# Kernel optimization log

Hardware: AMD Instinct MI355X
Metric: run time of the kernel (lower is better)

## Reference

```python
import jax, jax.numpy as jnp
import numpy as np

B, C, H, W = 4, 64, 128, 128
CO, K, PAD, STRIDE = 64, 3, 1, 1


def setup_inputs() -> dict:
    key = jax.random.key(0)
    k1, k2, k3 = jax.random.split(key, 3)
    x = jax.random.normal(k1, (B, C, H, W), dtype=jnp.float32)
    # small offset weights so predicted offsets stay near the regular grid
    w_off = jax.random.normal(k2, (2 * K * K, C, K, K), dtype=jnp.float32) * 0.01
    b_off = jnp.zeros((2 * K * K,), dtype=jnp.float32)
    w_def = jax.random.normal(k3, (CO, C, K, K), dtype=jnp.float32) * (1.0 / np.sqrt(C * K * K))
    return {"x": x, "w_off": w_off, "b_off": b_off, "w_def": w_def}


def _deform_forward(x, w_off, b_off, w_def):
    Bs, Cs, Hs, Ws = x.shape
    Co = w_def.shape[0]
    KK = K * K
    # offset conv: [B, 2*K*K, Ho, Wo]
    off = jax.lax.conv_general_dilated(
        x, w_off, (STRIDE, STRIDE), [(PAD, PAD), (PAD, PAD)],
        dimension_numbers=("NCHW", "OIHW", "NCHW"))
    off = off + b_off[None, :, None, None]
    Ho, Wo = off.shape[2], off.shape[3]
    off = off.reshape(Bs, KK, 2, Ho, Wo)  # channel 2k -> dy, 2k+1 -> dx
    ky = (jnp.arange(KK) // K).astype(x.dtype)
    kx = (jnp.arange(KK) % K).astype(x.dtype)
    gy = (jnp.arange(Ho) * STRIDE - PAD).astype(x.dtype)
    gx = (jnp.arange(Wo) * STRIDE - PAD).astype(x.dtype)
    # sampling positions per (batch, tap, out_y, out_x)
    py = off[:, :, 0] + ky[None, :, None, None] + gy[None, None, :, None]
    px = off[:, :, 1] + kx[None, :, None, None] + gx[None, None, None, :]
    y0 = jnp.floor(py)
    x0 = jnp.floor(px)
    dy = py - y0
    dx = px - x0
    y0i = y0.astype(jnp.int32)
    x0i = x0.astype(jnp.int32)
    xf = x.reshape(Bs, Cs, Hs * Ws)

    def gather(iy, ix):
        valid = (iy >= 0) & (iy < Hs) & (ix >= 0) & (ix < Ws)
        idx = jnp.clip(iy, 0, Hs - 1) * Ws + jnp.clip(ix, 0, Ws - 1)  # [B,KK,Ho,Wo]
        g = jax.vmap(lambda xb, ib: jnp.take(xb, ib.reshape(-1), axis=1))(xf, idx)
        g = g.reshape(Bs, Cs, KK, Ho, Wo)
        return g * valid[:, None].astype(x.dtype)

    # bilinear sample with zero padding outside the image (torchvision semantics)
    sampled = gather(y0i, x0i) * ((1 - dy) * (1 - dx))[:, None]
    sampled = sampled + gather(y0i, x0i + 1) * ((1 - dy) * dx)[:, None]
    sampled = sampled + gather(y0i + 1, x0i) * (dy * (1 - dx))[:, None]
    sampled = sampled + gather(y0i + 1, x0i + 1) * (dy * dx)[:, None]
    # conv-style weighted accumulation over (channel, tap)
    return jnp.einsum("bckhw,ock->bohw", sampled, w_def.reshape(Co, Cs, KK))


def reference(x, w_off, b_off, w_def):
    return _deform_forward(x, w_off, b_off, w_def)
```

## Files before the change

### kernel.cpp

```cpp
#include <hip/hip_runtime.h>
#include <math.h>


typedef short  v4s __attribute__((ext_vector_type(4)));
typedef short  v8s __attribute__((ext_vector_type(8)));
typedef float  v4f __attribute__((ext_vector_type(4)));
typedef float  v2f __attribute__((ext_vector_type(2)));

namespace {
constexpr int Bn = 4, Cn = 64, Hn = 128, Wn = 128, COn = 64;
constexpr int HWn = 16384;
constexpr int CKn = 576;
constexpr int TILE = 16;
constexpr int RS = 580;
constexpr int HW2 = 132;
constexpr int XPITCH = HW2 * 16;
constexpr size_t XH_OFF   = 0;
constexpr size_t ASWZ_OFF = 2230272;
constexpr size_t AOFF_OFF = ASWZ_OFF + 18432;
constexpr size_t OFFG_OFF = AOFF_OFF + 9216;
}

__device__ __forceinline__ unsigned short f2bf(float f) {
    union { float f; unsigned int u; } v; v.f = f;
    unsigned int u = v.u;
    u += 0x7fffu + ((u >> 16) & 1u);
    return (unsigned short)(u >> 16);
}
__device__ __forceinline__ unsigned int pack2bf(float a, float b) {
    return (unsigned int)f2bf(a) | ((unsigned int)f2bf(b) << 16);
}
__device__ __forceinline__ v2f unpk(unsigned int u) {
    v2f r;
    r.x = __uint_as_float(u << 16);
    r.y = __uint_as_float(u & 0xffff0000u);
    return r;
}

__global__ __launch_bounds__(256) void k_pre(const float* __restrict__ x,
                                             const float* __restrict__ w_def,
                                             const float* __restrict__ w_off,
                                             unsigned int* __restrict__ xh,
                                             unsigned short* __restrict__ aswz,
                                             unsigned short* __restrict__ aoff) {
    const int blk = blockIdx.x;
    const int tid = threadIdx.x;
    if (blk < 1024) {
        __shared__ float tile[64][65];
        const int lane = tid & 63;
        const int grp  = tid >> 6;
        const int b    = blk >> 8;
        const int hw0  = (blk & 255) << 6;
#pragma unroll
        for (int r = 0; r < 16; ++r) {
            const int c = (r << 2) + grp;
            tile[c][lane] = x[(b * Cn + c) * HWn + hw0 + lane];
        }
        __syncthreads();
        const int h = lane >> 5;
        const int m = lane & 31;
#pragma unroll
        for (int r = 0; r < 8; ++r) {
            const int hwl = (r << 3) + (grp << 1) + h;
            const int hw  = hw0 + hwl;
            const int yy  = hw >> 7;
            const int xx  = hw & (Wn - 1);
            const unsigned int u = pack2bf(tile[2 * m][hwl], tile[2 * m + 1][hwl]);
            xh[((size_t)(b * HW2 + yy + 2) * HW2 + (xx + 2)) * 32 + m] = u;
        }
    } else if (blk < 1240) {
        const int idx = (blk - 1024) * 256 + tid;
        if (idx < 36864) {
            const int j = idx & 7;
            const int l = (idx >> 3) & 63;
            const int s = (idx >> 9) % 18;
            const int r = idx / 9216;
            const int co = 16 * r + (l & 15);
            const int kk = 32 * s + 4 * (l >> 4) + (j & 3) + 16 * (j >> 2);
            const int tap = kk >> 6, c = kk & 63;
            aswz[idx] = f2bf(w_def[co * CKn + c * 9 + tap]);
        } else {
            const int i2 = idx - 36864;
            const int j = i2 & 7;
            const int l = (i2 >> 3) & 63;
            const int s = (i2 >> 9) % 18;
            const int r = i2 / 9216;
            const int co = 16 * r + (l & 15);
            const int kk = 32 * s + 4 * (l >> 4) + (j & 3) + 16 * (j >> 2);
            const int tap = kk >> 6, c = kk & 63;
            aoff[i2] = (co < 18) ? f2bf(w_off[co * CKn + c * 9 + tap]) : (unsigned short)0;
        }
    } else {
        const int i = (blk - 1240) * 256 + tid;
        const int b = i / 16640;
        const int r = i % 16640;
        int yy, xx, q;
        if (r < 8448) {
            const int y = r / 2112;
            yy = (y < 2) ? y : 128 + y;
            const int rem = r % 2112;
            xx = rem >> 4;
            q  = rem & 15;
        } else {
            const int r2 = r - 8448;
            yy = 2 + (r2 >> 6);
            const int rem = r2 & 63;
            const int xs = rem >> 4;
            xx = (xs < 2) ? xs : 128 + xs;
            q  = rem & 15;
        }
        ((uint2*)xh)[(((size_t)b * HW2 + yy) * HW2 + xx) * 16 + q] = make_uint2(0u, 0u);
    }
}

__global__ __launch_bounds__(256, 4) void k_offset(const uint2* __restrict__ xh2,
                                                   const unsigned short* __restrict__ aoff,
                                                   const float* __restrict__ b_off,
                                                   float* __restrict__ off_g) {
    __shared__ unsigned short Bl[TILE * RS];
    __shared__ float part[4][18][16];
    uint2* Bl2 = (uint2*)Bl;
    const int tid  = threadIdx.x;
    const int lane = tid & 63;
    const int wid  = tid >> 6;
    const int g    = lane >> 4;
    const int c15  = lane & 15;
    const int q    = lane & 15;
    const int pq   = lane >> 4;
    const int b    = blockIdx.x >> 10;
    const int p0   = (blockIdx.x & 1023) * TILE;
    const int pix  = (wid << 2) + pq;
    const int p    = p0 + pix;
    const int oy   = p >> 7;
    const int ox   = p & (Wn - 1);
    const int xbase = b * (HW2 * HW2 * 16);

#pragma unroll
    for (int k = 0; k < 9; ++k) {
        const int sy = oy + k / 3 - 1;
        const int sx = ox + k % 3 - 1;
        Bl2[pix * 145 + k * 16 + q] = xh2[xbase + ((sy + 2) * HW2 + (sx + 2)) * 16 + q];
    }
    __syncthreads();

    v4f pa0 = {0.f,0.f,0.f,0.f};
    v4f pa1 = {0.f,0.f,0.f,0.f};
    for (int s = wid; s < 18; s += 4) {
        const int kb = 32 * s + 4 * g;
        const unsigned short* b0p = &Bl[c15 * RS + kb];
        const v4s lo0 = *reinterpret_cast<const v4s*>(b0p);
        const v4s hi0 = *reinterpret_cast<const v4s*>(b0p + 16);
        const v8s bb0 = {lo0[0],lo0[1],lo0[2],lo0[3],hi0[0],hi0[1],hi0[2],hi0[3]};
        const v8s a0 = *reinterpret_cast<const v8s*>(aoff + (size_t)(0 * 18 + s) * 512 + lane * 8);
        const v8s a1 = *reinterpret_cast<const v8s*>(aoff + (size_t)(1 * 18 + s) * 512 + lane * 8);
        pa0 = __builtin_amdgcn_mfma_f32_16x16x32_bf16(a0, bb0, pa0, 0, 0, 0);
        pa1 = __builtin_amdgcn_mfma_f32_16x16x32_bf16(a1, bb0, pa1, 0, 0, 0);
    }
#pragma unroll
    for (int r = 0; r < 4; ++r) {
        const int co0 = (g << 2) + r;
        part[wid][co0][c15] = pa0[r];
        const int co1 = 16 + (g << 2) + r;
        if (co1 < 18)
            part[wid][co1][c15] = pa1[r];
    }
    __syncthreads();
    for (int idx = tid; idx < 288; idx += 256) {
        const int px = idx / 18, ch = idx % 18;
        off_g[((size_t)(b * HWn + p0)) * 18 + idx] =
            part[0][ch][px] + part[1][ch][px] + part[2][ch][px] + part[3][ch][px] + b_off[ch];
    }
}

__global__ __launch_bounds__(256, 4) void k_main(const uint2* __restrict__ xh2,
                                                 const float* __restrict__ off_g,
                                                 const unsigned short* __restrict__ aswz,
                                                 float* __restrict__ out) {
    __shared__ unsigned short Bl[TILE * RS];
    __shared__ float offl[16][18];
    uint2* Bl2 = (uint2*)Bl;
    const int tid  = threadIdx.x;
    const int lane = tid & 63;
    const int wid  = tid >> 6;
    const int g    = lane >> 4;
    const int c15  = lane & 15;
    const int q    = lane & 15;
    const int pq   = lane >> 4;
    const int b    = blockIdx.x >> 10;
    const int p0   = (blockIdx.x & 1023) * TILE;
    const int pix  = (wid << 2) + pq;
    const int p    = p0 + pix;
    const int oy   = p >> 7;
    const int ox   = p & (Wn - 1);
    const int xbase = b * (HW2 * HW2 * 16);

    for (int idx = tid; idx < 288; idx += 256)
        offl[idx / 18][idx % 18] = off_g[((size_t)(b * HWn + p0)) * 18 + idx];
    __syncthreads();

#pragma unroll
    for (int k = 0; k < 9; ++k) {
        const float py = offl[pix][2 * k]     + (float)(oy + k / 3 - 1);
        const float px = offl[pix][2 * k + 1] + (float)(ox + k % 3 - 1);
        const float fy = floorf(py);
        const float fx = floorf(px);
        const float ay = py - fy;
        const float ax = px - fx;
        int iy0 = (int)fy;
        int ix0 = (int)fx;
        iy0 = max(-2, min(iy0, 128));
        ix0 = max(-2, min(ix0, 128));
        const float w00 = (1.f - ay) * (1.f - ax);
        const float w01 = (1.f - ay) * ax;
        const float w10 = ay * (1.f - ax);
        const float w11 = ay * ax;
        const uint2* r0 = xh2 + xbase + ((iy0 + 2) * HW2 + (ix0 + 2)) * 16 + q;
        const uint2 u00 = r0[0];
        const uint2 u01 = r0[16];
        const uint2 u10 = r0[XPITCH];
        const uint2 u11 = r0[XPITCH + 16];
        v2f va = unpk(u00.x) * w00;
        va += unpk(u01.x) * w01;
        va += unpk(u10.x) * w10;
        va += unpk(u11.x) * w11;
        v2f vb = unpk(u00.y) * w00;
        vb += unpk(u01.y) * w01;
        vb += unpk(u10.y) * w10;
        vb += unpk(u11.y) * w11;
        Bl2[pix * 145 + k * 16 + q] = make_uint2(pack2bf(va.x, va.y), pack2bf(vb.x, vb.y));
    }
    __syncthreads();

    v4f acc0 = {0.f,0.f,0.f,0.f};
    const unsigned short* arow = aswz + (size_t)wid * 9216 + lane * 8;
#pragma unroll
    for (int s = 0; s < 18; ++s) {
        const v8s a = *reinterpret_cast<const v8s*>(arow + s * 512);
        const int kb = 32 * s + 4 * g;
        const unsigned short* b0p = &Bl[c15 * RS + kb];
        const v4s lo0 = *reinterpret_cast<const v4s*>(b0p);
        const v4s hi0 = *reinterpret_cast<const v4s*>(b0p + 16);
        const v8s bb0 = {lo0[0],lo0[1],lo0[2],lo0[3],hi0[0],hi0[1],hi0[2],hi0[3]};
        acc0 = __builtin_amdgcn_mfma_f32_16x16x32_bf16(a, bb0, acc0, 0, 0, 0);
    }
    const int co = (wid << 4) + (g << 2);
    float* op = out + ((size_t)(b * COn + co)) * HWn + p0 + c15;
#pragma unroll
    for (int r = 0; r < 4; ++r)
        op[(size_t)r * HWn] = acc0[r];
}

extern "C" void kernel_launch(void* const* d_in, const int* in_sizes, int n_in,
                              void* d_out, int out_size, void* d_ws, size_t ws_size,
                              hipStream_t stream) {
    const float* x     = (const float*)d_in[0];
    const float* w_off = (const float*)d_in[1];
    const float* b_off = (const float*)d_in[2];
    const float* w_def = (const float*)d_in[3];
    float* outp = (float*)d_out;
    float* wsf  = (float*)d_ws;
    unsigned int* xh = (unsigned int*)(wsf + XH_OFF);
    unsigned short* aswz = (unsigned short*)(wsf + ASWZ_OFF);
    unsigned short* aoff = (unsigned short*)(wsf + AOFF_OFF);
    float* off_g = wsf + OFFG_OFF;

    k_pre<<<1500, 256, 0, stream>>>(x, w_def, w_off, xh, aswz, aoff);
    k_offset<<<Bn * (HWn / TILE), 256, 0, stream>>>((const uint2*)xh, aoff, b_off, off_g);
    k_main<<<Bn * (HWn / TILE), 256, 0, stream>>>((const uint2*)xh, off_g, aswz, outp);
}
```

Before: 54.73 us.

## Restructure offset conv: per-wave pixel tiles loaded directly from global, drop LDS reduction

The offset-conv kernel now gives each wave its own 16 output pixels and has it walk the full 576-long reduction, loading MFMA B operands straight from the padded bf16 input in global memory. Before, the block staged a 16-pixel im2col tile in LDS and split the K loop across waves. This removes the LDS staging, both block barriers and the cross-wave partial-sum reduction. The block covers 64 pixels and the occupancy hint rises to 8 blocks. In exchange, each wave runs 18 serial MFMA pairs fed by scattered global loads instead of shared-memory reads, and writes its outputs directly with strided stores.

```diff
diff --git a/kernel.cpp b/kernel.cpp
--- a/kernel.cpp
+++ b/kernel.cpp
@@ -113,62 +113,49 @@
     }
 }
 
-__global__ __launch_bounds__(256, 4) void k_offset(const uint2* __restrict__ xh2,
+__global__ __launch_bounds__(256, 8) void k_offset(const uint2* __restrict__ xh2,
                                                    const unsigned short* __restrict__ aoff,
                                                    const float* __restrict__ b_off,
                                                    float* __restrict__ off_g) {
-    __shared__ unsigned short Bl[TILE * RS];
-    __shared__ float part[4][18][16];
-    uint2* Bl2 = (uint2*)Bl;
     const int tid  = threadIdx.x;
     const int lane = tid & 63;
     const int wid  = tid >> 6;
     const int g    = lane >> 4;
     const int c15  = lane & 15;
-    const int q    = lane & 15;
-    const int pq   = lane >> 4;
-    const int b    = blockIdx.x >> 10;
-    const int p0   = (blockIdx.x & 1023) * TILE;
-    const int pix  = (wid << 2) + pq;
-    const int p    = p0 + pix;
+    const int b    = blockIdx.x >> 8;
+    const int p0   = (blockIdx.x & 255) << 6;
+    const int p    = p0 + (wid << 4) + c15;
     const int oy   = p >> 7;
     const int ox   = p & (Wn - 1);
     const int xbase = b * (HW2 * HW2 * 16);
 
-#pragma unroll
-    for (int k = 0; k < 9; ++k) {
-        const int sy = oy + k / 3 - 1;
-        const int sx = ox + k % 3 - 1;
-        Bl2[pix * 145 + k * 16 + q] = xh2[xbase + ((sy + 2) * HW2 + (sx + 2)) * 16 + q];
-    }
-    __syncthreads();
-
     v4f pa0 = {0.f,0.f,0.f,0.f};
     v4f pa1 = {0.f,0.f,0.f,0.f};
-    for (int s = wid; s < 18; s += 4) {
-        const int kb = 32 * s + 4 * g;
-        const unsigned short* b0p = &Bl[c15 * RS + kb];
-        const v4s lo0 = *reinterpret_cast<const v4s*>(b0p);
-        const v4s hi0 = *reinterpret_cast<const v4s*>(b0p + 16);
-        const v8s bb0 = {lo0[0],lo0[1],lo0[2],lo0[3],hi0[0],hi0[1],hi0[2],hi0[3]};
+#pragma unroll
+    for (int s = 0; s < 18; ++s) {
+        const int tap = s >> 1;
+        const int sy  = oy + tap / 3 - 1;
+        const int sx  = ox + tap % 3 - 1;
+        const int qidx = ((s & 1) << 3) + g;
+        const uint2* ptr = xh2 + xbase + ((sy + 2) * HW2 + (sx + 2)) * 16 + qidx;
+        const uint2 lo = ptr[0];
+        const uint2 hi = ptr[4];
+        const v4s lo4 = *reinterpret_cast<const v4s*>(&lo);
+        const v4s hi4 = *reinterpret_cast<const v4s*>(&hi);
+        const v8s bb = {lo4[0],lo4[1],lo4[2],lo4[3],hi4[0],hi4[1],hi4[2],hi4[3]};
         const v8s a0 = *reinterpret_cast<const v8s*>(aoff + (size_t)(0 * 18 + s) * 512 + lane * 8);
         const v8s a1 = *reinterpret_cast<const v8s*>(aoff + (size_t)(1 * 18 + s) * 512 + lane * 8);
-        pa0 = __builtin_amdgcn_mfma_f32_16x16x32_bf16(a0, bb0, pa0, 0, 0, 0);
-        pa1 = __builtin_amdgcn_mfma_f32_16x16x32_bf16(a1, bb0, pa1, 0, 0, 0);
-    }
+        pa0 = __builtin_amdgcn_mfma_f32_16x16x32_bf16(a0, bb, pa0, 0, 0, 0);
+        pa1 = __builtin_amdgcn_mfma_f32_16x16x32_bf16(a1, bb, pa1, 0, 0, 0);
+    }
+    const size_t obase = (size_t)(b * HWn + p) * 18;
 #pragma unroll
     for (int r = 0; r < 4; ++r) {
         const int co0 = (g << 2) + r;
-        part[wid][co0][c15] = pa0[r];
+        off_g[obase + co0] = pa0[r] + b_off[co0];
         const int co1 = 16 + (g << 2) + r;
         if (co1 < 18)
-            part[wid][co1][c15] = pa1[r];
-    }
-    __syncthreads();
-    for (int idx = tid; idx < 288; idx += 256) {
-        const int px = idx / 18, ch = idx % 18;
-        off_g[((size_t)(b * HWn + p0)) * 18 + idx] =
-            part[0][ch][px] + part[1][ch][px] + part[2][ch][px] + part[3][ch][px] + b_off[ch];
+            off_g[obase + co1] = pa1[r] + b_off[co1];
     }
 }
 
@@ -265,6 +252,6 @@
     float* off_g = wsf + OFFG_OFF;
 
     k_pre<<<1500, 256, 0, stream>>>(x, w_def, w_off, xh, aswz, aoff);
-    k_offset<<<Bn * (HWn / TILE), 256, 0, stream>>>((const uint2*)xh, aoff, b_off, off_g);
+    k_offset<<<Bn * (HWn / 64), 256, 0, stream>>>((const uint2*)xh, aoff, b_off, off_g);
     k_main<<<Bn * (HWn / TILE), 256, 0, stream>>>((const uint2*)xh, off_g, aswz, outp);
 }
```

New measurement: 66.16 us. +20.9%, slower.
